# Optimization experiments

Hardware: AMD Instinct MI355X
Metric: run time of the kernel (lower is better)

Reference implementation:

```python
import jax, jax.numpy as jnp
import numpy as np

B, N, D, H = 2, 2048, 1024, 16
DH = D // H
DF = 4 * D
SCALE = D ** (-0.5)  # standard_scale=False -> dim**-0.5
EPS = 1e-5


def _ln(x, w, b):
    mu = jnp.mean(x, axis=-1, keepdims=True)
    var = jnp.mean(jnp.square(x - mu), axis=-1, keepdims=True)
    return (x - mu) * jax.lax.rsqrt(var + EPS) * w + b


def setup_inputs() -> dict:
    key = jax.random.key(0)
    ks = jax.random.split(key, 12)
    s = lambda fan_in: (1.0 / np.sqrt(fan_in))
    return {
        "x": jax.random.normal(ks[0], (B, N, D), jnp.float32),
        "gamma": jax.random.uniform(ks[1], (B, H), jnp.float32),
        "dist_matrix": jax.random.uniform(ks[2], (N, N), jnp.float32),
        "ln1_w": jnp.ones((D,), jnp.float32),
        "ln1_b": jnp.zeros((D,), jnp.float32),
        "qkv_w": jax.random.normal(ks[3], (D, 3 * D), jnp.float32) * s(D),
        "qkv_b": jnp.zeros((3 * D,), jnp.float32),
        "proj_w": jax.random.normal(ks[4], (D, D), jnp.float32) * s(D),
        "proj_b": jnp.zeros((D,), jnp.float32),
        "ln2_w": jnp.ones((D,), jnp.float32),
        "ln2_b": jnp.zeros((D,), jnp.float32),
        "mlp_w1": jax.random.normal(ks[5], (D, DF), jnp.float32) * s(D),
        "mlp_b1": jnp.zeros((DF,), jnp.float32),
        "mlp_w2": jax.random.normal(ks[6], (DF, D), jnp.float32) * s(DF),
        "mlp_b2": jnp.zeros((D,), jnp.float32),
    }


def reference(x, gamma, dist_matrix, ln1_w, ln1_b, qkv_w, qkv_b, proj_w, proj_b,
              ln2_w, ln2_b, mlp_w1, mlp_b1, mlp_w2, mlp_b2):
    # --- ZoomAttention on norm1(x) ---
    h = _ln(x, ln1_w, ln1_b)                                   # [B,N,D]
    qkv = h @ qkv_w + qkv_b                                    # [B,N,3D]
    qkv = qkv.reshape(B, N, 3, H, DH).transpose(2, 0, 3, 1, 4)  # [3,B,H,N,DH]
    q, k, v = qkv[0], qkv[1], qkv[2]
    scores = jnp.einsum("bhnd,bhmd->bhnm", q, k) * SCALE       # [B,H,N,N]
    scores = scores - gamma[:, :, None, None] * dist_matrix[None, None]
    attn = jax.nn.softmax(scores, axis=-1)
    out = jnp.einsum("bhnm,bhmd->bhnd", attn, v)               # [B,H,N,DH]
    out = out.transpose(0, 2, 1, 3).reshape(B, N, D)
    x = x + (out @ proj_w + proj_b)
    # --- MLP (exact GELU, torch default) ---
    h2 = _ln(x, ln2_w, ln2_b)
    h2 = jax.nn.gelu(h2 @ mlp_w1 + mlp_b1, approximate=False) @ mlp_w2 + mlp_b2
    return x + h2
```

## Files before the change

### kernel.cpp

```cpp
#include <hip/hip_runtime.h>
#include <hip/hip_bf16.h>


#define SCALE_ 0.03125f
#define EPS_   1e-5f
#define LOG2E_ 1.4426950408889634f
#define SC2_   (SCALE_ * LOG2E_)

typedef unsigned short u16;
typedef __attribute__((ext_vector_type(8))) short short8;
typedef __attribute__((ext_vector_type(4))) float f32x4;
typedef __attribute__((ext_vector_type(16))) float f32x16;
typedef __attribute__((ext_vector_type(4))) unsigned short u16x4;

__device__ inline float b2f(u16 u){ unsigned x = ((unsigned)u) << 16; float f; __builtin_memcpy(&f, &x, 4); return f; }
__device__ inline u16 f2b(float f){ __hip_bfloat16 h = __float2bfloat16(f); u16 u; __builtin_memcpy(&u, &h, 2); return u; }

__device__ inline void glds16(const u16* g, u16* l) {
    __builtin_amdgcn_global_load_lds(
        (const __attribute__((address_space(1))) void*)g,
        (__attribute__((address_space(3))) void*)l, 16, 0, 0);
}

__device__ inline unsigned cvtpk(float a, float b) {
    unsigned r;
    asm("v_cvt_pk_bf16_f32 %0, %1, %2" : "=v"(r) : "v"(a), "v"(b));
    return r;
}
__device__ inline void pl32swap(unsigned &a, unsigned &b) {
    asm("v_permlane32_swap_b32 %0, %1" : "+v"(a), "+v"(b));
}
__device__ inline short8 mk8(unsigned a, unsigned b, unsigned c, unsigned d) {
    union { unsigned u[4]; short8 s; } x;
    x.u[0] = a; x.u[1] = b; x.u[2] = c; x.u[3] = d;
    return x.s;
}

__global__ __launch_bounds__(256) void transpose_cast(const float* __restrict__ src,
                                                      u16* __restrict__ dst, int K, int N) {
    __shared__ float t[32][33];
    int nb = blockIdx.x * 32, kb = blockIdx.y * 32;
    int tx = threadIdx.x & 31, ty = threadIdx.x >> 5;
    for (int i = 0; i < 4; i++) {
        int r = ty + i * 8;
        t[r][tx] = src[(size_t)(kb + r) * N + nb + tx];
    }
    __syncthreads();
    for (int i = 0; i < 4; i++) {
        int r = ty + i * 8;
        dst[(size_t)(nb + r) * K + kb + tx] = f2b(t[tx][r]);
    }
}

__global__ __launch_bounds__(256) void cast_scale_bf16(const float* __restrict__ src,
                                                       u16* __restrict__ dst, int n4, float scale) {
    int i = blockIdx.x * 256 + threadIdx.x;
    if (i < n4) {
        float4 v = ((const float4*)src)[i];
        u16x4 o;
        o[0] = f2b(v.x * scale); o[1] = f2b(v.y * scale);
        o[2] = f2b(v.z * scale); o[3] = f2b(v.w * scale);
        ((u16x4*)dst)[i] = o;
    }
}

__global__ __launch_bounds__(256) void ln_bf16(const float* __restrict__ x,
                                               const float* __restrict__ w,
                                               const float* __restrict__ b,
                                               u16* __restrict__ out) {
    int row = blockIdx.x, t = threadIdx.x;
    float4 v = ((const float4*)(x + (size_t)row * 1024))[t];
    float s1 = v.x + v.y + v.z + v.w;
    float s2 = v.x * v.x + v.y * v.y + v.z * v.z + v.w * v.w;
    for (int o = 32; o > 0; o >>= 1) { s1 += __shfl_xor(s1, o); s2 += __shfl_xor(s2, o); }
    __shared__ float a1[4], a2[4];
    if ((t & 63) == 0) { a1[t >> 6] = s1; a2[t >> 6] = s2; }
    __syncthreads();
    s1 = a1[0] + a1[1] + a1[2] + a1[3];
    s2 = a2[0] + a2[1] + a2[2] + a2[3];
    float mu = s1 * (1.0f / 1024.0f);
    float var = s2 * (1.0f / 1024.0f) - mu * mu;
    float rs = rsqrtf(var + EPS_);
    float4 wv = ((const float4*)w)[t];
    float4 bv = ((const float4*)b)[t];
    u16x4 o;
    o[0] = f2b((v.x - mu) * rs * wv.x + bv.x);
    o[1] = f2b((v.y - mu) * rs * wv.y + bv.y);
    o[2] = f2b((v.z - mu) * rs * wv.z + bv.z);
    o[3] = f2b((v.w - mu) * rs * wv.w + bv.w);
    ((u16x4*)(out + (size_t)row * 1024))[t] = o;
}

template <int MODE>
__global__ __launch_bounds__(512) void gemm256_8ph(
    const u16* __restrict__ A, const u16* __restrict__ Bt,
    const float* __restrict__ bias, int K,
    u16* __restrict__ outb,
    u16* __restrict__ qp, u16* __restrict__ kp, u16* __restrict__ vtp) {
    __shared__ u16 LS[4][2][256 * 32];
    int tid = threadIdx.x;
    int w = tid >> 6, lane = tid & 63, g = lane >> 4, ln = lane & 15;
    int wr = w >> 2, wc = w & 3;
    int gx = gridDim.x;
    int nwg = gx * gridDim.y;
    int lin = blockIdx.y * gx + blockIdx.x;
    int swz = (lin & 7) * (nwg >> 3) + (lin >> 3);
    int bx = swz % gx, by = swz / gx;
    int br = by * 256, bc = bx * 256;
    int jx = (((lane & 3) ^ ((lane >> 3) & 3)) << 3);
    const u16* Ast = A + (size_t)(br + w * 32 + (lane >> 2)) * K + jx;
    const u16* Bst = Bt + (size_t)(bc + w * 32 + (lane >> 2)) * K + jx;
    size_t r16 = (size_t)16 * K;
    const int ldsW = (w * 32) * 32;
    f32x4 acc[8][4] = {};
    int NT = K >> 5;
    int slotr = ((g ^ ((ln >> 1) & 3)) << 3);
    for (int kt = 0; kt < 3; ++kt) {
        glds16(Ast + (size_t)kt * 32, &LS[kt][0][ldsW]);
        glds16(Ast + (size_t)kt * 32 + r16, &LS[kt][0][ldsW + 512]);
        glds16(Bst + (size_t)kt * 32, &LS[kt][1][ldsW]);
        glds16(Bst + (size_t)kt * 32 + r16, &LS[kt][1][ldsW + 512]);
    }
    asm volatile("s_waitcnt vmcnt(8)" ::: "memory");
    __builtin_amdgcn_s_barrier();
    short8 aa[4], bb[4];
    for (int kt = 0; kt < NT; ++kt) {
        const u16* bufA = &LS[kt & 3][0][0];
        const u16* bufB = &LS[kt & 3][1][0];
        int s3 = kt + 3;
        #pragma unroll
        for (int m = 0; m < 4; ++m)
            aa[m] = *(const short8*)&bufA[(wr * 128 + m * 16 + ln) * 32 + slotr];
        #pragma unroll
        for (int n = 0; n < 4; ++n)
            bb[n] = *(const short8*)&bufB[(wc * 64 + n * 16 + ln) * 32 + slotr];
        if (s3 < NT) {
            u16* d = &LS[s3 & 3][0][ldsW];
            glds16(Ast + (size_t)s3 * 32, d);
            glds16(Ast + (size_t)s3 * 32 + r16, d + 512);
        }
        __builtin_amdgcn_s_barrier();
        asm volatile("s_waitcnt lgkmcnt(0)" ::: "memory");
        __builtin_amdgcn_sched_barrier(0);
        __builtin_amdgcn_s_setprio(1);
        #pragma unroll
        for (int m = 0; m < 4; ++m)
            #pragma unroll
            for (int n = 0; n < 4; ++n)
                acc[m][n] = __builtin_amdgcn_mfma_f32_16x16x32_bf16(aa[m], bb[n], acc[m][n], 0, 0, 0);
        __builtin_amdgcn_s_setprio(0);
        __builtin_amdgcn_sched_barrier(0);
        __builtin_amdgcn_s_barrier();
        #pragma unroll
        for (int m = 0; m < 4; ++m)
            aa[m] = *(const short8*)&bufA[(wr * 128 + 64 + m * 16 + ln) * 32 + slotr];
        if (s3 < NT) {
            u16* d = &LS[s3 & 3][1][ldsW];
            glds16(Bst + (size_t)s3 * 32, d);
            glds16(Bst + (size_t)s3 * 32 + r16, d + 512);
        }
        if (kt + 3 < NT)      asm volatile("s_waitcnt vmcnt(8)" ::: "memory");
        else if (kt + 2 < NT) asm volatile("s_waitcnt vmcnt(4)" ::: "memory");
        else if (kt + 1 < NT) asm volatile("s_waitcnt vmcnt(0)" ::: "memory");
        __builtin_amdgcn_s_barrier();
        asm volatile("s_waitcnt lgkmcnt(0)" ::: "memory");
        __builtin_amdgcn_sched_barrier(0);
        __builtin_amdgcn_s_setprio(1);
        #pragma unroll
        for (int m = 0; m < 4; ++m)
            #pragma unroll
            for (int n = 0; n < 4; ++n)
                acc[4 + m][n] = __builtin_amdgcn_mfma_f32_16x16x32_bf16(aa[m], bb[n], acc[4 + m][n], 0, 0, 0);
        __builtin_amdgcn_s_setprio(0);
        __builtin_amdgcn_sched_barrier(0);
        __builtin_amdgcn_s_barrier();
    }
    #pragma unroll
    for (int m = 0; m < 8; ++m) {
        int row0 = br + wr * 128 + m * 16 + g * 4;
        #pragma unroll
        for (int n = 0; n < 4; ++n) {
            int col = bc + wc * 64 + n * 16 + ln;
            float bv = bias[col];
            if constexpr (MODE == 0) {
                int which = col >> 10, cc = col & 1023, hh = cc >> 6, dh = cc & 63;
                int bb2 = row0 >> 11, nn0 = row0 & 2047;
                size_t bh = (size_t)(bb2 * 16 + hh);
                if (which == 0) {
                    for (int r = 0; r < 4; r++)
                        qp[((bh * 2048 + nn0 + r) << 6) + dh] = f2b((acc[m][n][r] + bv) * SC2_);
                } else if (which == 1) {
                    for (int r = 0; r < 4; r++)
                        kp[((bh * 2048 + nn0 + r) << 6) + dh] = f2b(acc[m][n][r] + bv);
                } else {
                    u16x4 o;
                    for (int r = 0; r < 4; r++) o[r] = f2b(acc[m][n][r] + bv);
                    *(u16x4*)&vtp[((bh * 64 + dh) << 11) + nn0] = o;
                }
            } else {
                for (int r = 0; r < 4; r++) {
                    float v = acc[m][n][r] + bv;
                    float gl = 0.5f * v * (1.0f + erff(v * 0.7071067811865476f));
                    outb[(size_t)(row0 + r) * 4096 + col] = f2b(gl);
                }
            }
        }
    }
}

template <int MODE, int BN>
__global__ __launch_bounds__(256) void gemm_bf16(
    const u16* __restrict__ A, const u16* __restrict__ Bt,
    const float* __restrict__ bias, int M, int N, int K,
    const float* __restrict__ res, float* __restrict__ outf) {
    constexpr int NN = BN / 32;
    __shared__ u16 As[128 * 64];
    __shared__ u16 Bs[BN * 64];
    int br = blockIdx.y * 128, bc = blockIdx.x * BN;
    int tid = threadIdx.x;
    int w = tid >> 6, lane = tid & 63, g = lane >> 4, ln = lane & 15;
    int wr = (w >> 1) * 64, wc = (w & 1) * (BN / 2);
    f32x4 acc[4][NN] = {};
    int sgcol = (((lane & 7) ^ (lane >> 3)) << 3);
    int arow = w * 32 + (lane >> 3);
    int brow = w * (BN / 4) + (lane >> 3);
    const u16* Ap = A + (size_t)(br + arow) * K + sgcol;
    const u16* Bp = Bt + (size_t)(bc + brow) * K + sgcol;
    u16* lA = &As[(w * 32) * 64];
    u16* lB = &Bs[(w * (BN / 4)) * 64];
    size_t rstep = (size_t)8 * K;
    for (int kt = 0; kt < K; kt += 64) {
        __syncthreads();
        #pragma unroll
        for (int i = 0; i < 4; i++) glds16(Ap + kt + i * rstep, lA + i * 512);
        #pragma unroll
        for (int i = 0; i < BN / 32; i++) glds16(Bp + kt + i * rstep, lB + i * 512);
        __syncthreads();
        #pragma unroll
        for (int kk = 0; kk < 2; kk++) {
            int so = (((kk << 2) + g) ^ (ln & 7)) << 3;
            short8 af[4], bfr[NN];
            #pragma unroll
            for (int m = 0; m < 4; m++)  af[m]  = *(const short8*)&As[(wr + m * 16 + ln) * 64 + so];
            #pragma unroll
            for (int n = 0; n < NN; n++) bfr[n] = *(const short8*)&Bs[(wc + n * 16 + ln) * 64 + so];
            #pragma unroll
            for (int m = 0; m < 4; m++)
                #pragma unroll
                for (int n = 0; n < NN; n++)
                    acc[m][n] = __builtin_amdgcn_mfma_f32_16x16x32_bf16(af[m], bfr[n], acc[m][n], 0, 0, 0);
        }
    }
    #pragma unroll
    for (int m = 0; m < 4; m++) {
        int row0 = br + wr + m * 16 + g * 4;
        #pragma unroll
        for (int n = 0; n < NN; n++) {
            int col = bc + wc + n * 16 + ln;
            float bv = bias[col];
            if constexpr (MODE == 1) {
                for (int r = 0; r < 4; r++) {
                    size_t idx = (size_t)(row0 + r) * 1024 + col;
                    outf[idx] = res[idx] + acc[m][n][r] + bv;
                }
            } else {
                for (int r = 0; r < 4; r++) {
                    size_t idx = (size_t)(row0 + r) * 1024 + col;
                    outf[idx] = outf[idx] + acc[m][n][r] + bv;
                }
            }
        }
    }
}

__global__ __launch_bounds__(256) void attn_fwd32(
    const u16* __restrict__ qg, const u16* __restrict__ kg, const u16* __restrict__ vtg,
    const u16* __restrict__ distb, const float* __restrict__ gamma, u16* __restrict__ ao) {
    __shared__ u16 Ks[2][64 * 64];
    __shared__ u16 Vs[2][64 * 64];
    int qt = blockIdx.x, bh = blockIdx.y;
    int b = bh >> 4, h16 = bh & 15;
    int tid = threadIdx.x, w = tid >> 6, lane = tid & 63;
    int ln = lane & 31, hh = lane >> 5;
    float gam = gamma[bh];
    int qglob = qt * 128 + w * 32 + ln;
    const u16* qrow = qg + ((size_t)bh * 2048 + qglob) * 64;
    short8 qB[4];
    #pragma unroll
    for (int st = 0; st < 4; ++st) qB[st] = *(const short8*)(qrow + st * 16 + hh * 8);
    const u16* drow = distb + (size_t)qglob * 2048 + hh * 4;
    int srow = w * 16 + (lane >> 3);
    int sgc = (((lane & 7) ^ ((lane >> 3) & 7)) << 3);
    const u16* kst = kg + ((size_t)bh * 2048 + srow) * 64 + sgc;
    const u16* vst = vtg + ((size_t)bh * 64 + srow) * 2048 + sgc;
    u16* lk0 = &Ks[0][(w * 16) * 64]; u16* lk1 = &Ks[1][(w * 16) * 64];
    u16* lv0 = &Vs[0][(w * 16) * 64]; u16* lv1 = &Vs[1][(w * 16) * 64];
    glds16(kst, lk0); glds16(kst + 512, lk0 + 512);
    glds16(vst, lv0); glds16(vst + 16384, lv0 + 512);
    __syncthreads();
    float m2 = -3.0e38f, lsum = 0.0f;
    f32x16 acc0 = {}, acc1 = {};
    int cur = 0;
    for (int kt = 0; kt < 32; ++kt) {
        if (kt < 31) {
            u16* dk = cur ? lk0 : lk1;
            u16* dvp = cur ? lv0 : lv1;
            const u16* ks = kst + (size_t)(kt + 1) * 4096;
            const u16* vs = vst + (size_t)(kt + 1) * 64;
            glds16(ks, dk); glds16(ks + 512, dk + 512);
            glds16(vs, dvp); glds16(vs + 16384, dvp + 512);
        }
        u16x4 dd[8];
        #pragma unroll
        for (int i = 0; i < 8; ++i)
            dd[i] = *(const u16x4*)(drow + kt * 64 + (i >> 2) * 32 + (i & 3) * 8);
        const u16* KB = &Ks[cur][0];
        const u16* VB = &Vs[cur][0];
        f32x16 sa0 = {}, sa1 = {};
        __builtin_amdgcn_s_setprio(1);
        #pragma unroll
        for (int st = 0; st < 4; ++st) {
            int so = (((st * 2 + hh) ^ (ln & 7)) << 3);
            short8 kf0 = *(const short8*)&KB[ln * 64 + so];
            short8 kf1 = *(const short8*)&KB[(32 + ln) * 64 + so];
            sa0 = __builtin_amdgcn_mfma_f32_32x32x16_bf16(kf0, qB[st], sa0, 0, 0, 0);
            sa1 = __builtin_amdgcn_mfma_f32_32x32x16_bf16(kf1, qB[st], sa1, 0, 0, 0);
        }
        __builtin_amdgcn_s_setprio(0);
        float p0[16], p1[16];
        float pm = -3.0e38f;
        #pragma unroll
        for (int r = 0; r < 16; ++r) {
            p0[r] = sa0[r] - gam * b2f(dd[r >> 2][r & 3]);
            p1[r] = sa1[r] - gam * b2f(dd[4 + (r >> 2)][r & 3]);
            pm = fmaxf(pm, fmaxf(p0[r], p1[r]));
        }
        pm = fmaxf(pm, __shfl_xor(pm, 32));
        if (!__all(pm - m2 <= 8.0f)) {
            float nm = fmaxf(m2, pm);
            float al = __builtin_exp2f(m2 - nm);
            m2 = nm;
            lsum *= al;
            acc0 *= al; acc1 *= al;
        }
        float ps = 0.0f;
        #pragma unroll
        for (int r = 0; r < 16; ++r) {
            p0[r] = __builtin_exp2f(p0[r] - m2); ps += p0[r];
            p1[r] = __builtin_exp2f(p1[r] - m2); ps += p1[r];
        }
        lsum += ps;
        unsigned w0[8], w1[8];
        #pragma unroll
        for (int qr = 0; qr < 4; ++qr) {
            w0[qr * 2]     = cvtpk(p0[qr * 4], p0[qr * 4 + 1]);
            w0[qr * 2 + 1] = cvtpk(p0[qr * 4 + 2], p0[qr * 4 + 3]);
            w1[qr * 2]     = cvtpk(p1[qr * 4], p1[qr * 4 + 1]);
            w1[qr * 2 + 1] = cvtpk(p1[qr * 4 + 2], p1[qr * 4 + 3]);
        }
        pl32swap(w0[0], w0[2]); pl32swap(w0[1], w0[3]);
        pl32swap(w0[4], w0[6]); pl32swap(w0[5], w0[7]);
        pl32swap(w1[0], w1[2]); pl32swap(w1[1], w1[3]);
        pl32swap(w1[4], w1[6]); pl32swap(w1[5], w1[7]);
        short8 pB[4];
        pB[0] = mk8(w0[0], w0[1], w0[2], w0[3]);
        pB[1] = mk8(w0[4], w0[5], w0[6], w0[7]);
        pB[2] = mk8(w1[0], w1[1], w1[2], w1[3]);
        pB[3] = mk8(w1[4], w1[5], w1[6], w1[7]);
        __builtin_amdgcn_s_setprio(1);
        #pragma unroll
        for (int sg = 0; sg < 4; ++sg) {
            int so = (((sg * 2 + hh) ^ (ln & 7)) << 3);
            short8 vf0 = *(const short8*)&VB[ln * 64 + so];
            short8 vf1 = *(const short8*)&VB[(32 + ln) * 64 + so];
            acc0 = __builtin_amdgcn_mfma_f32_32x32x16_bf16(vf0, pB[sg], acc0, 0, 0, 0);
            acc1 = __builtin_amdgcn_mfma_f32_32x32x16_bf16(vf1, pB[sg], acc1, 0, 0, 0);
        }
        __builtin_amdgcn_s_setprio(0);
        __syncthreads();
        cur ^= 1;
    }
    lsum += __shfl_xor(lsum, 32);
    float inv = 1.0f / lsum;
    u16* aop = ao + ((size_t)(b * 2048 + qglob)) * 1024 + h16 * 64 + hh * 4;
    #pragma unroll
    for (int qr = 0; qr < 4; ++qr) {
        u16x4 o0, o1;
        #pragma unroll
        for (int r = 0; r < 4; ++r) {
            o0[r] = f2b(acc0[qr * 4 + r] * inv);
            o1[r] = f2b(acc1[qr * 4 + r] * inv);
        }
        *(u16x4*)(aop + qr * 8) = o0;
        *(u16x4*)(aop + 32 + qr * 8) = o1;
    }
}

extern "C" void kernel_launch(void* const* d_in, const int* in_sizes, int n_in,
                              void* d_out, int out_size, void* d_ws, size_t ws_size,
                              hipStream_t stream) {
    const float* x     = (const float*)d_in[0];
    const float* gamma = (const float*)d_in[1];
    const float* dist  = (const float*)d_in[2];
    const float* ln1w  = (const float*)d_in[3];
    const float* ln1b  = (const float*)d_in[4];
    const float* qkvw  = (const float*)d_in[5];
    const float* qkvb  = (const float*)d_in[6];
    const float* projw = (const float*)d_in[7];
    const float* projb = (const float*)d_in[8];
    const float* ln2w  = (const float*)d_in[9];
    const float* ln2b  = (const float*)d_in[10];
    const float* w1    = (const float*)d_in[11];
    const float* b1    = (const float*)d_in[12];
    const float* w2    = (const float*)d_in[13];
    const float* b2    = (const float*)d_in[14];
    float* out = (float*)d_out;
    char* ws = (char*)d_ws;
    u16* wqkvT  = (u16*)(ws + 0);
    u16* wprojT = (u16*)(ws + 6291456);
    u16* w1T    = (u16*)(ws + 8388608);
    u16* w2T    = (u16*)(ws + 16777216);
    u16* distb  = (u16*)(ws + 25165824);
    u16* hb     = (u16*)(ws + 33554432);
    u16* qb     = (u16*)(ws + 41943040);
    u16* kb     = (u16*)(ws + 50331648);
    u16* vtb    = (u16*)(ws + 58720256);
    u16* aob    = (u16*)(ws + 67108864);
    u16* gb     = hb;
    u16* h2b    = aob;

    dim3 blk(256);
    transpose_cast<<<dim3(3072 / 32, 1024 / 32), blk, 0, stream>>>(qkvw, wqkvT, 1024, 3072);
    transpose_cast<<<dim3(1024 / 32, 1024 / 32), blk, 0, stream>>>(projw, wprojT, 1024, 1024);
    transpose_cast<<<dim3(4096 / 32, 1024 / 32), blk, 0, stream>>>(w1, w1T, 1024, 4096);
    transpose_cast<<<dim3(1024 / 32, 4096 / 32), blk, 0, stream>>>(w2, w2T, 4096, 1024);
    cast_scale_bf16<<<4096, blk, 0, stream>>>(dist, distb, 2048 * 2048 / 4, LOG2E_);
    ln_bf16<<<4096, blk, 0, stream>>>(x, ln1w, ln1b, hb);
    gemm256_8ph<0><<<dim3(12, 16), dim3(512), 0, stream>>>(hb, wqkvT, qkvb, 1024,
                                                           nullptr, qb, kb, vtb);
    attn_fwd32<<<dim3(16, 32), blk, 0, stream>>>(qb, kb, vtb, distb, gamma, aob);
    gemm_bf16<1, 64><<<dim3(16, 32), blk, 0, stream>>>(aob, wprojT, projb, 4096, 1024, 1024,
                                                       x, out);
    ln_bf16<<<4096, blk, 0, stream>>>(out, ln2w, ln2b, h2b);
    gemm256_8ph<2><<<dim3(16, 16), dim3(512), 0, stream>>>(h2b, w1T, b1, 1024,
                                                           gb, nullptr, nullptr, nullptr);
    gemm_bf16<3, 64><<<dim3(16, 32), blk, 0, stream>>>(gb, w2T, b2, 4096, 1024, 4096,
                                                       nullptr, out);
}
```

Measured before the change: 304.4 us.

## Split attention keys across warp pairs with register-direct K/V loads and merge

Rewrites the attention kernel so each block handles 64 queries with two warp groups that each process half of the key range (split-K flash attention). The groups then merge their partial softmax state through shared memory. K and V fragments are loaded straight from global memory into registers, with K prefetched one tile ahead, which removes the LDS staging and the per-iteration barriers. The grid grows to 1024 blocks with a swizzled block-to-tile mapping and launch bounds requesting 3 blocks per CU. The trade-off is redundant, less coalesced global loads of K/V per warp, more register pressure, and an extra merge step.

```diff
diff --git a/kernel.cpp b/kernel.cpp
--- a/kernel.cpp
+++ b/kernel.cpp
@@ -273,60 +273,61 @@
     }
 }
 
-__global__ __launch_bounds__(256) void attn_fwd32(
+__global__ __launch_bounds__(256, 3) void attn_reg(
     const u16* __restrict__ qg, const u16* __restrict__ kg, const u16* __restrict__ vtg,
     const u16* __restrict__ distb, const float* __restrict__ gamma, u16* __restrict__ ao) {
-    __shared__ u16 Ks[2][64 * 64];
-    __shared__ u16 Vs[2][64 * 64];
-    int qt = blockIdx.x, bh = blockIdx.y;
+    __shared__ float mrg[2][64][34];
+    int id = blockIdx.x;
+    int L = (id & 7) * 128 + (id >> 3);
+    int bh = L >> 5, qgp = L & 31;
     int b = bh >> 4, h16 = bh & 15;
-    int tid = threadIdx.x, w = tid >> 6, lane = tid & 63;
+    int tid = threadIdx.x;
+    int w2 = tid >> 7, qs = (tid >> 6) & 1, lane = tid & 63;
     int ln = lane & 31, hh = lane >> 5;
     float gam = gamma[bh];
-    int qglob = qt * 128 + w * 32 + ln;
+    int qglob = qgp * 64 + qs * 32 + ln;
     const u16* qrow = qg + ((size_t)bh * 2048 + qglob) * 64;
     short8 qB[4];
     #pragma unroll
     for (int st = 0; st < 4; ++st) qB[st] = *(const short8*)(qrow + st * 16 + hh * 8);
-    const u16* drow = distb + (size_t)qglob * 2048 + hh * 4;
-    int srow = w * 16 + (lane >> 3);
-    int sgc = (((lane & 7) ^ ((lane >> 3) & 7)) << 3);
-    const u16* kst = kg + ((size_t)bh * 2048 + srow) * 64 + sgc;
-    const u16* vst = vtg + ((size_t)bh * 64 + srow) * 2048 + sgc;
-    u16* lk0 = &Ks[0][(w * 16) * 64]; u16* lk1 = &Ks[1][(w * 16) * 64];
-    u16* lv0 = &Vs[0][(w * 16) * 64]; u16* lv1 = &Vs[1][(w * 16) * 64];
-    glds16(kst, lk0); glds16(kst + 512, lk0 + 512);
-    glds16(vst, lv0); glds16(vst + 16384, lv0 + 512);
-    __syncthreads();
+    const u16* kbase = kg + ((size_t)(bh * 2048 + w2 * 1024)) * 64 + hh * 8;
+    const u16* vbase = vtg + ((size_t)bh * 64) * 2048 + w2 * 1024 + hh * 8;
+    const u16* drow = distb + (size_t)qglob * 2048 + w2 * 1024 + hh * 4;
     float m2 = -3.0e38f, lsum = 0.0f;
     f32x16 acc0 = {}, acc1 = {};
-    int cur = 0;
-    for (int kt = 0; kt < 32; ++kt) {
-        if (kt < 31) {
-            u16* dk = cur ? lk0 : lk1;
-            u16* dvp = cur ? lv0 : lv1;
-            const u16* ks = kst + (size_t)(kt + 1) * 4096;
-            const u16* vs = vst + (size_t)(kt + 1) * 64;
-            glds16(ks, dk); glds16(ks + 512, dk + 512);
-            glds16(vs, dvp); glds16(vs + 16384, dvp + 512);
-        }
+    short8 kf[8];
+    #pragma unroll
+    for (int st = 0; st < 4; ++st) {
+        kf[st]     = *(const short8*)(kbase + (size_t)ln * 64 + st * 16);
+        kf[4 + st] = *(const short8*)(kbase + (size_t)(32 + ln) * 64 + st * 16);
+    }
+    for (int kt = 0; kt < 16; ++kt) {
         u16x4 dd[8];
         #pragma unroll
         for (int i = 0; i < 8; ++i)
             dd[i] = *(const u16x4*)(drow + kt * 64 + (i >> 2) * 32 + (i & 3) * 8);
-        const u16* KB = &Ks[cur][0];
-        const u16* VB = &Vs[cur][0];
+        short8 vf[8];
+        #pragma unroll
+        for (int sg = 0; sg < 4; ++sg) {
+            vf[sg]     = *(const short8*)(vbase + (size_t)ln * 2048 + kt * 64 + sg * 16);
+            vf[4 + sg] = *(const short8*)(vbase + (size_t)(32 + ln) * 2048 + kt * 64 + sg * 16);
+        }
         f32x16 sa0 = {}, sa1 = {};
         __builtin_amdgcn_s_setprio(1);
         #pragma unroll
         for (int st = 0; st < 4; ++st) {
-            int so = (((st * 2 + hh) ^ (ln & 7)) << 3);
-            short8 kf0 = *(const short8*)&KB[ln * 64 + so];
-            short8 kf1 = *(const short8*)&KB[(32 + ln) * 64 + so];
-            sa0 = __builtin_amdgcn_mfma_f32_32x32x16_bf16(kf0, qB[st], sa0, 0, 0, 0);
-            sa1 = __builtin_amdgcn_mfma_f32_32x32x16_bf16(kf1, qB[st], sa1, 0, 0, 0);
+            sa0 = __builtin_amdgcn_mfma_f32_32x32x16_bf16(kf[st], qB[st], sa0, 0, 0, 0);
+            sa1 = __builtin_amdgcn_mfma_f32_32x32x16_bf16(kf[4 + st], qB[st], sa1, 0, 0, 0);
         }
         __builtin_amdgcn_s_setprio(0);
+        if (kt < 15) {
+            const u16* kn = kbase + (size_t)(kt + 1) * 64 * 64;
+            #pragma unroll
+            for (int st = 0; st < 4; ++st) {
+                kf[st]     = *(const short8*)(kn + (size_t)ln * 64 + st * 16);
+                kf[4 + st] = *(const short8*)(kn + (size_t)(32 + ln) * 64 + st * 16);
+            }
+        }
         float p0[16], p1[16];
         float pm = -3.0e38f;
         #pragma unroll
@@ -370,29 +371,40 @@
         __builtin_amdgcn_s_setprio(1);
         #pragma unroll
         for (int sg = 0; sg < 4; ++sg) {
-            int so = (((sg * 2 + hh) ^ (ln & 7)) << 3);
-            short8 vf0 = *(const short8*)&VB[ln * 64 + so];
-            short8 vf1 = *(const short8*)&VB[(32 + ln) * 64 + so];
-            acc0 = __builtin_amdgcn_mfma_f32_32x32x16_bf16(vf0, pB[sg], acc0, 0, 0, 0);
-            acc1 = __builtin_amdgcn_mfma_f32_32x32x16_bf16(vf1, pB[sg], acc1, 0, 0, 0);
+            acc0 = __builtin_amdgcn_mfma_f32_32x32x16_bf16(vf[sg], pB[sg], acc0, 0, 0, 0);
+            acc1 = __builtin_amdgcn_mfma_f32_32x32x16_bf16(vf[4 + sg], pB[sg], acc1, 0, 0, 0);
         }
         __builtin_amdgcn_s_setprio(0);
-        __syncthreads();
-        cur ^= 1;
     }
     lsum += __shfl_xor(lsum, 32);
-    float inv = 1.0f / lsum;
-    u16* aop = ao + ((size_t)(b * 2048 + qglob)) * 1024 + h16 * 64 + hh * 4;
-    #pragma unroll
-    for (int qr = 0; qr < 4; ++qr) {
-        u16x4 o0, o1;
-        #pragma unroll
-        for (int r = 0; r < 4; ++r) {
-            o0[r] = f2b(acc0[qr * 4 + r] * inv);
-            o1[r] = f2b(acc1[qr * 4 + r] * inv);
-        }
-        *(u16x4*)(aop + qr * 8) = o0;
-        *(u16x4*)(aop + 32 + qr * 8) = o1;
+    if (w2 == 1) {
+        #pragma unroll
+        for (int r = 0; r < 16; ++r) {
+            mrg[qs][lane][r] = acc0[r];
+            mrg[qs][lane][16 + r] = acc1[r];
+        }
+        mrg[qs][lane][32] = m2;
+        mrg[qs][lane][33] = lsum;
+    }
+    __syncthreads();
+    if (w2 == 0) {
+        float m1 = mrg[qs][lane][32], l1 = mrg[qs][lane][33];
+        float M = fmaxf(m2, m1);
+        float s0 = __builtin_exp2f(m2 - M);
+        float s1 = __builtin_exp2f(m1 - M);
+        float inv = 1.0f / (lsum * s0 + l1 * s1);
+        u16* aop = ao + ((size_t)(b * 2048 + qglob)) * 1024 + h16 * 64 + hh * 4;
+        #pragma unroll
+        for (int qr = 0; qr < 4; ++qr) {
+            u16x4 o0, o1;
+            #pragma unroll
+            for (int r = 0; r < 4; ++r) {
+                o0[r] = f2b((acc0[qr * 4 + r] * s0 + mrg[qs][lane][qr * 4 + r] * s1) * inv);
+                o1[r] = f2b((acc1[qr * 4 + r] * s0 + mrg[qs][lane][16 + qr * 4 + r] * s1) * inv);
+            }
+            *(u16x4*)(aop + qr * 8) = o0;
+            *(u16x4*)(aop + 32 + qr * 8) = o1;
+        }
     }
 }
 
@@ -438,7 +450,7 @@
     ln_bf16<<<4096, blk, 0, stream>>>(x, ln1w, ln1b, hb);
     gemm256_8ph<0><<<dim3(12, 16), dim3(512), 0, stream>>>(hb, wqkvT, qkvb, 1024,
                                                            nullptr, qb, kb, vtb);
-    attn_fwd32<<<dim3(16, 32), blk, 0, stream>>>(qb, kb, vtb, distb, gamma, aob);
+    attn_reg<<<dim3(1024), blk, 0, stream>>>(qb, kb, vtb, distb, gamma, aob);
     gemm_bf16<1, 64><<<dim3(16, 32), blk, 0, stream>>>(aob, wprojT, projb, 4096, 1024, 1024,
                                                        x, out);
     ln_bf16<<<4096, blk, 0, stream>>>(out, ln2w, ln2b, h2b);
```

After: 422.6 us. 38.8% more time.

## Split attention keys across two wave groups and read fp32 distance directly

Applied to the files above, without the earlier changes.

Each attention block now runs 512 threads. Two groups of four waves each handle one half of the key sequence for the same 128 queries. At the end the partial softmax states (max, sum, accumulators) are merged through shared memory. The separate kernel that cast the distance matrix to bf16 is dropped; attention reads the fp32 dist matrix directly and folds log2e into gamma. This removes a full pass over the 16MB dist matrix and doubles the waves per block, at the cost of twice the distance-read bandwidth inside attention, doubled LDS, and a merge step.

```diff
diff --git a/kernel.cpp b/kernel.cpp
--- a/kernel.cpp
+++ b/kernel.cpp
@@ -49,18 +49,6 @@
     for (int i = 0; i < 4; i++) {
         int r = ty + i * 8;
         dst[(size_t)(nb + r) * K + kb + tx] = f2b(t[tx][r]);
-    }
-}
-
-__global__ __launch_bounds__(256) void cast_scale_bf16(const float* __restrict__ src,
-                                                       u16* __restrict__ dst, int n4, float scale) {
-    int i = blockIdx.x * 256 + threadIdx.x;
-    if (i < n4) {
-        float4 v = ((const float4*)src)[i];
-        u16x4 o;
-        o[0] = f2b(v.x * scale); o[1] = f2b(v.y * scale);
-        o[2] = f2b(v.z * scale); o[3] = f2b(v.w * scale);
-        ((u16x4*)dst)[i] = o;
     }
 }
 
@@ -273,49 +261,46 @@
     }
 }
 
-__global__ __launch_bounds__(256) void attn_fwd32(
+__global__ __launch_bounds__(512, 4) void attn_fwd(
     const u16* __restrict__ qg, const u16* __restrict__ kg, const u16* __restrict__ vtg,
-    const u16* __restrict__ distb, const float* __restrict__ gamma, u16* __restrict__ ao) {
-    __shared__ u16 Ks[2][64 * 64];
-    __shared__ u16 Vs[2][64 * 64];
+    const float* __restrict__ dist, const float* __restrict__ gamma, u16* __restrict__ ao) {
+    __shared__ u16 Ks[2][2][64 * 64];
+    __shared__ u16 Vs[2][2][64 * 64];
     int qt = blockIdx.x, bh = blockIdx.y;
     int b = bh >> 4, h16 = bh & 15;
     int tid = threadIdx.x, w = tid >> 6, lane = tid & 63;
+    int kh = w >> 2, qs = w & 3;
     int ln = lane & 31, hh = lane >> 5;
-    float gam = gamma[bh];
-    int qglob = qt * 128 + w * 32 + ln;
+    float gam = gamma[bh] * LOG2E_;
+    int qglob = qt * 128 + qs * 32 + ln;
     const u16* qrow = qg + ((size_t)bh * 2048 + qglob) * 64;
     short8 qB[4];
     #pragma unroll
     for (int st = 0; st < 4; ++st) qB[st] = *(const short8*)(qrow + st * 16 + hh * 8);
-    const u16* drow = distb + (size_t)qglob * 2048 + hh * 4;
-    int srow = w * 16 + (lane >> 3);
-    int sgc = (((lane & 7) ^ ((lane >> 3) & 7)) << 3);
-    const u16* kst = kg + ((size_t)bh * 2048 + srow) * 64 + sgc;
-    const u16* vst = vtg + ((size_t)bh * 64 + srow) * 2048 + sgc;
-    u16* lk0 = &Ks[0][(w * 16) * 64]; u16* lk1 = &Ks[1][(w * 16) * 64];
-    u16* lv0 = &Vs[0][(w * 16) * 64]; u16* lv1 = &Vs[1][(w * 16) * 64];
-    glds16(kst, lk0); glds16(kst + 512, lk0 + 512);
-    glds16(vst, lv0); glds16(vst + 16384, lv0 + 512);
+    const float* drow = dist + (size_t)qglob * 2048 + kh * 1024 + hh * 4;
+    int l3 = lane >> 3, l7 = lane & 7;
+    int swsl = ((l7 ^ (l3 & 7)) << 3);
+    const u16* kbase = kg + ((size_t)(bh * 2048 + kh * 1024 + qs * 16 + l3)) * 64 + swsl;
+    const u16* vbase = vtg + ((size_t)(bh * 64 + qs * 16 + l3)) * 2048 + kh * 1024 + swsl;
+    u16* lk0 = &Ks[kh][0][(qs * 16) * 64]; u16* lk1 = &Ks[kh][1][(qs * 16) * 64];
+    u16* lv0 = &Vs[kh][0][(qs * 16) * 64]; u16* lv1 = &Vs[kh][1][(qs * 16) * 64];
+    glds16(kbase, lk0); glds16(kbase + 512, lk0 + 512);
+    glds16(vbase, lv0); glds16(vbase + 16384, lv0 + 512);
     __syncthreads();
     float m2 = -3.0e38f, lsum = 0.0f;
     f32x16 acc0 = {}, acc1 = {};
     int cur = 0;
-    for (int kt = 0; kt < 32; ++kt) {
-        if (kt < 31) {
+    for (int kt = 0; kt < 16; ++kt) {
+        if (kt < 15) {
+            const u16* kn = kbase + (size_t)(kt + 1) * 4096;
+            const u16* vn = vbase + (size_t)(kt + 1) * 64;
             u16* dk = cur ? lk0 : lk1;
-            u16* dvp = cur ? lv0 : lv1;
-            const u16* ks = kst + (size_t)(kt + 1) * 4096;
-            const u16* vs = vst + (size_t)(kt + 1) * 64;
-            glds16(ks, dk); glds16(ks + 512, dk + 512);
-            glds16(vs, dvp); glds16(vs + 16384, dvp + 512);
-        }
-        u16x4 dd[8];
-        #pragma unroll
-        for (int i = 0; i < 8; ++i)
-            dd[i] = *(const u16x4*)(drow + kt * 64 + (i >> 2) * 32 + (i & 3) * 8);
-        const u16* KB = &Ks[cur][0];
-        const u16* VB = &Vs[cur][0];
+            u16* dv = cur ? lv0 : lv1;
+            glds16(kn, dk); glds16(kn + 512, dk + 512);
+            glds16(vn, dv); glds16(vn + 16384, dv + 512);
+        }
+        const u16* KB = &Ks[kh][cur][0];
+        const u16* VB = &Vs[kh][cur][0];
         f32x16 sa0 = {}, sa1 = {};
         __builtin_amdgcn_s_setprio(1);
         #pragma unroll
@@ -327,13 +312,25 @@
             sa1 = __builtin_amdgcn_mfma_f32_32x32x16_bf16(kf1, qB[st], sa1, 0, 0, 0);
         }
         __builtin_amdgcn_s_setprio(0);
-        float p0[16], p1[16];
+        const float* dt = drow + kt * 64;
         float pm = -3.0e38f;
         #pragma unroll
-        for (int r = 0; r < 16; ++r) {
-            p0[r] = sa0[r] - gam * b2f(dd[r >> 2][r & 3]);
-            p1[r] = sa1[r] - gam * b2f(dd[4 + (r >> 2)][r & 3]);
-            pm = fmaxf(pm, fmaxf(p0[r], p1[r]));
+        for (int i = 0; i < 4; ++i) {
+            f32x4 dv = *(const f32x4*)(dt + i * 8);
+            sa0[i * 4 + 0] -= gam * dv[0];
+            sa0[i * 4 + 1] -= gam * dv[1];
+            sa0[i * 4 + 2] -= gam * dv[2];
+            sa0[i * 4 + 3] -= gam * dv[3];
+            pm = fmaxf(pm, fmaxf(fmaxf(sa0[i*4], sa0[i*4+1]), fmaxf(sa0[i*4+2], sa0[i*4+3])));
+        }
+        #pragma unroll
+        for (int i = 0; i < 4; ++i) {
+            f32x4 dv = *(const f32x4*)(dt + 32 + i * 8);
+            sa1[i * 4 + 0] -= gam * dv[0];
+            sa1[i * 4 + 1] -= gam * dv[1];
+            sa1[i * 4 + 2] -= gam * dv[2];
+            sa1[i * 4 + 3] -= gam * dv[3];
+            pm = fmaxf(pm, fmaxf(fmaxf(sa1[i*4], sa1[i*4+1]), fmaxf(sa1[i*4+2], sa1[i*4+3])));
         }
         pm = fmaxf(pm, __shfl_xor(pm, 32));
         if (!__all(pm - m2 <= 8.0f)) {
@@ -346,17 +343,17 @@
         float ps = 0.0f;
         #pragma unroll
         for (int r = 0; r < 16; ++r) {
-            p0[r] = __builtin_exp2f(p0[r] - m2); ps += p0[r];
-            p1[r] = __builtin_exp2f(p1[r] - m2); ps += p1[r];
+            sa0[r] = __builtin_exp2f(sa0[r] - m2); ps += sa0[r];
+            sa1[r] = __builtin_exp2f(sa1[r] - m2); ps += sa1[r];
         }
         lsum += ps;
         unsigned w0[8], w1[8];
         #pragma unroll
         for (int qr = 0; qr < 4; ++qr) {
-            w0[qr * 2]     = cvtpk(p0[qr * 4], p0[qr * 4 + 1]);
-            w0[qr * 2 + 1] = cvtpk(p0[qr * 4 + 2], p0[qr * 4 + 3]);
-            w1[qr * 2]     = cvtpk(p1[qr * 4], p1[qr * 4 + 1]);
-            w1[qr * 2 + 1] = cvtpk(p1[qr * 4 + 2], p1[qr * 4 + 3]);
+            w0[qr * 2]     = cvtpk(sa0[qr * 4], sa0[qr * 4 + 1]);
+            w0[qr * 2 + 1] = cvtpk(sa0[qr * 4 + 2], sa0[qr * 4 + 3]);
+            w1[qr * 2]     = cvtpk(sa1[qr * 4], sa1[qr * 4 + 1]);
+            w1[qr * 2 + 1] = cvtpk(sa1[qr * 4 + 2], sa1[qr * 4 + 3]);
         }
         pl32swap(w0[0], w0[2]); pl32swap(w0[1], w0[3]);
         pl32swap(w0[4], w0[6]); pl32swap(w0[5], w0[7]);
@@ -381,18 +378,33 @@
         cur ^= 1;
     }
     lsum += __shfl_xor(lsum, 32);
-    float inv = 1.0f / lsum;
-    u16* aop = ao + ((size_t)(b * 2048 + qglob)) * 1024 + h16 * 64 + hh * 4;
-    #pragma unroll
-    for (int qr = 0; qr < 4; ++qr) {
-        u16x4 o0, o1;
-        #pragma unroll
-        for (int r = 0; r < 4; ++r) {
-            o0[r] = f2b(acc0[qr * 4 + r] * inv);
-            o1[r] = f2b(acc1[qr * 4 + r] * inv);
-        }
-        *(u16x4*)(aop + qr * 8) = o0;
-        *(u16x4*)(aop + 32 + qr * 8) = o1;
+    float* mrg = (float*)&Ks[0][0][0];
+    if (kh == 1) {
+        float* p = mrg + (size_t)(qs * 64 + lane) * 34;
+        #pragma unroll
+        for (int r = 0; r < 16; ++r) { p[r] = acc0[r]; p[16 + r] = acc1[r]; }
+        p[32] = m2; p[33] = lsum;
+    }
+    __syncthreads();
+    if (kh == 0) {
+        const float* p = mrg + (size_t)(qs * 64 + lane) * 34;
+        float m1 = p[32], l1 = p[33];
+        float M = fmaxf(m2, m1);
+        float s0 = __builtin_exp2f(m2 - M);
+        float s1 = __builtin_exp2f(m1 - M);
+        float inv = 1.0f / (lsum * s0 + l1 * s1);
+        u16* aop = ao + ((size_t)(b * 2048 + qglob)) * 1024 + h16 * 64 + hh * 4;
+        #pragma unroll
+        for (int qr = 0; qr < 4; ++qr) {
+            u16x4 o0, o1;
+            #pragma unroll
+            for (int r = 0; r < 4; ++r) {
+                o0[r] = f2b((acc0[qr * 4 + r] * s0 + p[qr * 4 + r] * s1) * inv);
+                o1[r] = f2b((acc1[qr * 4 + r] * s0 + p[16 + qr * 4 + r] * s1) * inv);
+            }
+            *(u16x4*)(aop + qr * 8) = o0;
+            *(u16x4*)(aop + 32 + qr * 8) = o1;
+        }
     }
 }
 
@@ -420,7 +432,6 @@
     u16* wprojT = (u16*)(ws + 6291456);
     u16* w1T    = (u16*)(ws + 8388608);
     u16* w2T    = (u16*)(ws + 16777216);
-    u16* distb  = (u16*)(ws + 25165824);
     u16* hb     = (u16*)(ws + 33554432);
     u16* qb     = (u16*)(ws + 41943040);
     u16* kb     = (u16*)(ws + 50331648);
@@ -434,11 +445,10 @@
     transpose_cast<<<dim3(1024 / 32, 1024 / 32), blk, 0, stream>>>(projw, wprojT, 1024, 1024);
     transpose_cast<<<dim3(4096 / 32, 1024 / 32), blk, 0, stream>>>(w1, w1T, 1024, 4096);
     transpose_cast<<<dim3(1024 / 32, 4096 / 32), blk, 0, stream>>>(w2, w2T, 4096, 1024);
-    cast_scale_bf16<<<4096, blk, 0, stream>>>(dist, distb, 2048 * 2048 / 4, LOG2E_);
     ln_bf16<<<4096, blk, 0, stream>>>(x, ln1w, ln1b, hb);
     gemm256_8ph<0><<<dim3(12, 16), dim3(512), 0, stream>>>(hb, wqkvT, qkvb, 1024,
                                                            nullptr, qb, kb, vtb);
-    attn_fwd32<<<dim3(16, 32), blk, 0, stream>>>(qb, kb, vtb, distb, gamma, aob);
+    attn_fwd<<<dim3(16, 32), dim3(512), 0, stream>>>(qb, kb, vtb, dist, gamma, aob);
     gemm_bf16<1, 64><<<dim3(16, 32), blk, 0, stream>>>(aob, wprojT, projb, 4096, 1024, 1024,
                                                        x, out);
     ln_bf16<<<4096, blk, 0, stream>>>(out, ln2w, ln2b, h2b);
```

Result: faster. 291.9 us (-4.1%).
